# Optimization experiments

Measured on AMD Instinct MI355X. Metric: run time of the kernel, lower is better.

## Reference

```python
import jax, jax.numpy as jnp
import numpy as np

T = 1048576          # number of time steps in the trace
SIGMA_NUM = 8
EPSILON_NUM = 8
FEAT = 2 + SIGMA_NUM + EPSILON_NUM  # [t, r_obs, sigmas..., epsilons...]


def setup_inputs() -> dict:
    key = jax.random.key(0)
    ks = jax.random.split(key, 6)
    trace = jax.random.normal(ks[0], (T, FEAT), dtype=jnp.float32)
    # column 0 is time: sorted grid with small dt so the 1M-step recurrence stays bounded
    trace = trace.at[:, 0].set(jnp.arange(T, dtype=jnp.float32) * 1e-3)
    # column 1 row 0 is the initial rate; keep it positive-ish
    trace = trace.at[0, 1].set(0.05)
    sigma_W = jax.random.normal(ks[1], (1, SIGMA_NUM), dtype=jnp.float32) * 0.01
    sigma_b = jax.random.normal(ks[2], (1,), dtype=jnp.float32) * 0.01
    eps_W = jax.random.normal(ks[3], (1, EPSILON_NUM), dtype=jnp.float32) * 0.01
    k = jnp.abs(jax.random.normal(ks[4], (1,), dtype=jnp.float32)) * 0.1
    theta = jnp.abs(jax.random.normal(ks[5], (1,), dtype=jnp.float32)) * 0.05
    return {"trace_data": trace, "sigma_W": sigma_W, "sigma_b": sigma_b,
            "eps_W": eps_W, "k": k, "theta": theta}


def reference(trace_data, sigma_W, sigma_b, eps_W, k, theta):
    S, E = SIGMA_NUM, EPSILON_NUM
    t = trace_data[:, 0]
    dts = t[1:] - t[:-1]                                   # [T-1]
    # sigma/epsilon projections depend only on trace data -> vectorize outside scan
    sig = trace_data[:-1, 2:2 + S] @ sigma_W[0] + sigma_b[0]   # [T-1]
    eps = trace_data[:-1, 2 + S:2 + S + E] @ eps_W[0]          # [T-1]
    kk = k[0]
    th = theta[0]
    r0 = trace_data[0, 1]

    def step(r, x):
        dt, s, e = x
        ode = r + kk * (th - r) * dt
        sde = s * jnp.sqrt(jnp.abs(r * dt)) * e
        r_next = ode + sde
        return r_next, r_next

    _, r_predicts = jax.lax.scan(step, r0, (dts, sig, eps))   # [T-1]
    regs = 2.0 * kk * th - sig ** 2                           # [T-1]
    return r_predicts, regs, dts
```

## Files before the change

### kernel.cpp

```cpp
#include <hip/hip_runtime.h>
#include <math.h>

#define NSTEPS  1048575
#define NPAD    1048576
#define FEAT    18
#define CLEN    4
#define CHUNKS  (NPAD / CLEN)
#define K2B     256
#define K2T     1024

__global__ void prep_kernel(const float* __restrict__ trace,
                            const float* __restrict__ sW, const float* __restrict__ sb,
                            const float* __restrict__ eW, const float* __restrict__ kp,
                            const float* __restrict__ thp,
                            float2* __restrict__ dc, float* __restrict__ seeds,
                            float* __restrict__ out, unsigned int* __restrict__ cnt)
{
    int n = blockIdx.x * blockDim.x + threadIdx.x;
    if (n == 0) *cnt = 0;
    if (n >= NSTEPS) { dc[n] = make_float2(0.f, 0.f); return; }
    const float2* r2 = (const float2*)(trace + (long)n * FEAT);
    float2 e0 = r2[0], e1 = r2[1], e2 = r2[2], e3 = r2[3], e4 = r2[4];
    float2 e5 = r2[5], e6 = r2[6], e7 = r2[7], e8 = r2[8];
    float tn1 = trace[(long)(n + 1) * FEAT];
    float d = tn1 - e0.x;
    float sig = sb[0];
    sig = fmaf(e1.x, sW[0], sig); sig = fmaf(e1.y, sW[1], sig);
    sig = fmaf(e2.x, sW[2], sig); sig = fmaf(e2.y, sW[3], sig);
    sig = fmaf(e3.x, sW[4], sig); sig = fmaf(e3.y, sW[5], sig);
    sig = fmaf(e4.x, sW[6], sig); sig = fmaf(e4.y, sW[7], sig);
    float ep = 0.f;
    ep = fmaf(e5.x, eW[0], ep); ep = fmaf(e5.y, eW[1], ep);
    ep = fmaf(e6.x, eW[2], ep); ep = fmaf(e6.y, eW[3], ep);
    ep = fmaf(e7.x, eW[4], ep); ep = fmaf(e7.y, eW[5], ep);
    ep = fmaf(e8.x, eW[6], ep); ep = fmaf(e8.y, eW[7], ep);
    float k = kp[0], th = thp[0];
    dc[n] = make_float2(d, sig * ep * sqrtf(fabsf(d)));
    out[NSTEPS + n]     = fmaf(-sig, sig, 2.f * k * th);
    out[2 * NSTEPS + n] = d;
    if ((n & 3) == 0)
        seeds[n >> 2] = th + (trace[1] - th) * __expf(-k * (e0.x - trace[0]));
}

#define GSTEP(dd, cc) { \
    float a   = fmaf(-k, (dd), 1.f); \
    float b   = kth * (dd); \
    float ar  = fabsf(r); \
    float sq  = sqrtf(ar); \
    float inv = (ar > 1e-30f) ? rsqrtf(ar) : 0.f; \
    float g   = fmaf(0.5f * (cc), copysignf(inv, r), a); \
    r = fmaf((cc), sq, fmaf(a, r, b)); \
    P *= g; }

#define FSTEP(dd, cc) { \
    float a = fmaf(-k, (dd), 1.f); \
    float b = kth * (dd); \
    rr = fmaf((cc), sqrtf(fabsf(rr)), fmaf(a, rr, b)); }

__device__ __forceinline__ void wave_scan_affine(float& A, float& B, int lane) {
#pragma unroll
    for (int d = 1; d < 64; d <<= 1) {
        float pA = __shfl_up(A, d, 64);
        float pB = __shfl_up(B, d, 64);
        if (lane >= d) { B = fmaf(A, pB, B); A *= pA; }
    }
}

__global__ void __launch_bounds__(K2T) fused_pass(
    const float2* __restrict__ dc, const float* __restrict__ seeds,
    const float* __restrict__ trace,
    const float* __restrict__ kp, const float* __restrict__ thp,
    float* __restrict__ out,
    float* __restrict__ gA, float* __restrict__ gB,
    unsigned int* __restrict__ cnt)
{
    __shared__ float wAs[16], wBs[16];
    __shared__ float sgA[K2B], sgB[K2B];
    const int tid = threadIdx.x, lane = tid & 63, wid = tid >> 6, bid = blockIdx.x;
    const int c = bid * K2T + tid;
    const float k = kp[0], th = thp[0], kth = k * th;
    const float4 q0 = ((const float4*)dc)[2 * c];
    const float4 q1 = ((const float4*)dc)[2 * c + 1];
    const float s = seeds[c];

    float r = s, P = 1.f;
    GSTEP(q0.x, q0.y)
    GSTEP(q0.z, q0.w)
    GSTEP(q1.x, q1.y)
    GSTEP(q1.z, q1.w)
    float A = P, B = fmaf(-P, s, r);

    float iA = A, iB = B;
    wave_scan_affine(iA, iB, lane);
    if (lane == 63) { wAs[wid] = iA; wBs[wid] = iB; }
    __syncthreads();
    if (wid == 0) {
        float aA = (lane < 16) ? wAs[lane] : 1.f;
        float aB = (lane < 16) ? wBs[lane] : 0.f;
        wave_scan_affine(aA, aB, lane);
        if (lane < 16) { wAs[lane] = aA; wBs[lane] = aB; }
    }
    __syncthreads();
    float weA = 1.f, weB = 0.f;
    if (wid > 0) { weA = wAs[wid - 1]; weB = wBs[wid - 1]; }
    float eA = __shfl_up(iA, 1, 64), eB = __shfl_up(iB, 1, 64);
    if (lane == 0) { eA = 1.f; eB = 0.f; }
    float Ate = eA * weA;
    float Bte = fmaf(eA, weB, eB);

    if (tid == 0) {
        __hip_atomic_store(&gA[bid], wAs[15], __ATOMIC_RELAXED, __HIP_MEMORY_SCOPE_AGENT);
        __hip_atomic_store(&gB[bid], wBs[15], __ATOMIC_RELAXED, __HIP_MEMORY_SCOPE_AGENT);
        __hip_atomic_fetch_add(cnt, 1u, __ATOMIC_ACQ_REL, __HIP_MEMORY_SCOPE_AGENT);
        while (__hip_atomic_load(cnt, __ATOMIC_ACQUIRE, __HIP_MEMORY_SCOPE_AGENT) < K2B)
            __builtin_amdgcn_s_sleep(1);
    }
    __syncthreads();

    if (tid < K2B) {
        sgA[tid] = __hip_atomic_load(&gA[tid], __ATOMIC_RELAXED, __HIP_MEMORY_SCOPE_AGENT);
        sgB[tid] = __hip_atomic_load(&gB[tid], __ATOMIC_RELAXED, __HIP_MEMORY_SCOPE_AGENT);
    }
    __syncthreads();
    for (int d = 1; d < K2B; d <<= 1) {
        float pA = 1.f, pB = 0.f;
        bool act = (tid < K2B) && (tid >= d);
        if (act) { pA = sgA[tid - d]; pB = sgB[tid - d]; }
        __syncthreads();
        if (act) { sgB[tid] = fmaf(sgA[tid], pB, sgB[tid]); sgA[tid] *= pA; }
        __syncthreads();
    }
    float beA = 1.f, beB = 0.f;
    if (bid > 0) { beA = sgA[bid - 1]; beB = sgB[bid - 1]; }

    float FA = Ate * beA;
    float FB = fmaf(Ate, beB, Bte);
    float rr = fmaf(FA, trace[1], FB);
    float4 ov;
    FSTEP(q0.x, q0.y) ov.x = rr;
    FSTEP(q0.z, q0.w) ov.y = rr;
    FSTEP(q1.x, q1.y) ov.z = rr;
    FSTEP(q1.z, q1.w) ov.w = rr;
    int nb = 4 * c;
    if (nb + 4 <= NSTEPS) {
        *(float4*)(out + nb) = ov;
    } else {
        out[nb + 0] = ov.x;
        out[nb + 1] = ov.y;
        out[nb + 2] = ov.z;
    }
}

extern "C" void kernel_launch(void* const* d_in, const int* in_sizes, int n_in,
                              void* d_out, int out_size, void* d_ws, size_t ws_size,
                              hipStream_t stream)
{
    const float* trace = (const float*)d_in[0];
    const float* sW    = (const float*)d_in[1];
    const float* sb    = (const float*)d_in[2];
    const float* eW    = (const float*)d_in[3];
    const float* kp    = (const float*)d_in[4];
    const float* thp   = (const float*)d_in[5];
    float* out = (float*)d_out;

    float*        w     = (float*)d_ws;
    float2*       dc    = (float2*)w;
    float*        seeds = w + 2 * NPAD;
    float*        gA    = seeds + CHUNKS;
    float*        gB    = gA + K2B;
    unsigned int* cnt   = (unsigned int*)(gB + K2B);

    prep_kernel<<<NPAD / 256, 256, 0, stream>>>(trace, sW, sb, eW, kp, thp,
                                                dc, seeds, out, cnt);
    fused_pass<<<K2B, K2T, 0, stream>>>(dc, seeds, trace, kp, thp, out, gA, gB, cnt);
}
```

Baseline: 130.7 us.

## Fuse prep into scan kernel with double-buffered LDS staging of trace rows

```diff
diff --git a/kernel.cpp b/kernel.cpp
--- a/kernel.cpp
+++ b/kernel.cpp
@@ -2,44 +2,31 @@
 #include <math.h>
 
 #define NSTEPS  1048575
-#define NPAD    1048576
 #define FEAT    18
-#define CLEN    4
-#define CHUNKS  (NPAD / CLEN)
-#define K2B     256
-#define K2T     1024
-
-__global__ void prep_kernel(const float* __restrict__ trace,
-                            const float* __restrict__ sW, const float* __restrict__ sb,
-                            const float* __restrict__ eW, const float* __restrict__ kp,
-                            const float* __restrict__ thp,
-                            float2* __restrict__ dc, float* __restrict__ seeds,
-                            float* __restrict__ out, unsigned int* __restrict__ cnt)
+#define NB      256
+#define NT      1024
+#define RPB     (NT * 4)
+#define CROWS   NT
+#define NCHUNK  (RPB / CROWS)
+#define CF4     ((CROWS * FEAT) / 4)
+
+#define GLDS16(g, l) \
+    __builtin_amdgcn_global_load_lds((const __attribute__((address_space(1))) void*)(g), \
+                                     (__attribute__((address_space(3))) void*)(l), 16, 0, 0)
+
+__device__ __forceinline__ void stage_chunk(const float* __restrict__ trace,
+                                            long gbase, float* dst, int tid)
 {
-    int n = blockIdx.x * blockDim.x + threadIdx.x;
-    if (n == 0) *cnt = 0;
-    if (n >= NSTEPS) { dc[n] = make_float2(0.f, 0.f); return; }
-    const float2* r2 = (const float2*)(trace + (long)n * FEAT);
-    float2 e0 = r2[0], e1 = r2[1], e2 = r2[2], e3 = r2[3], e4 = r2[4];
-    float2 e5 = r2[5], e6 = r2[6], e7 = r2[7], e8 = r2[8];
-    float tn1 = trace[(long)(n + 1) * FEAT];
-    float d = tn1 - e0.x;
-    float sig = sb[0];
-    sig = fmaf(e1.x, sW[0], sig); sig = fmaf(e1.y, sW[1], sig);
-    sig = fmaf(e2.x, sW[2], sig); sig = fmaf(e2.y, sW[3], sig);
-    sig = fmaf(e3.x, sW[4], sig); sig = fmaf(e3.y, sW[5], sig);
-    sig = fmaf(e4.x, sW[6], sig); sig = fmaf(e4.y, sW[7], sig);
-    float ep = 0.f;
-    ep = fmaf(e5.x, eW[0], ep); ep = fmaf(e5.y, eW[1], ep);
-    ep = fmaf(e6.x, eW[2], ep); ep = fmaf(e6.y, eW[3], ep);
-    ep = fmaf(e7.x, eW[4], ep); ep = fmaf(e7.y, eW[5], ep);
-    ep = fmaf(e8.x, eW[6], ep); ep = fmaf(e8.y, eW[7], ep);
-    float k = kp[0], th = thp[0];
-    dc[n] = make_float2(d, sig * ep * sqrtf(fabsf(d)));
-    out[NSTEPS + n]     = fmaf(-sig, sig, 2.f * k * th);
-    out[2 * NSTEPS + n] = d;
-    if ((n & 3) == 0)
-        seeds[n >> 2] = th + (trace[1] - th) * __expf(-k * (e0.x - trace[0]));
+    const float4* src = (const float4*)(trace + gbase * FEAT);
+#pragma unroll
+    for (int r = 0; r < 4; ++r) {
+        int i = r * NT + tid;
+        GLDS16(src + i, dst + i * 4);
+    }
+    if (tid < (CF4 - 4 * NT)) {
+        int i = 4 * NT + tid;
+        GLDS16(src + i, dst + i * 4);
+    }
 }
 
 #define GSTEP(dd, cc) { \
@@ -66,31 +53,91 @@
     }
 }
 
-__global__ void __launch_bounds__(K2T) fused_pass(
-    const float2* __restrict__ dc, const float* __restrict__ seeds,
+__global__ void __launch_bounds__(NT) cir_fused(
     const float* __restrict__ trace,
-    const float* __restrict__ kp, const float* __restrict__ thp,
+    const float* __restrict__ sW, const float* __restrict__ sb,
+    const float* __restrict__ eW, const float* __restrict__ kp,
+    const float* __restrict__ thp,
     float* __restrict__ out,
     float* __restrict__ gA, float* __restrict__ gB,
     unsigned int* __restrict__ cnt)
 {
+    __shared__ __align__(16) float  buf[2][CROWS * FEAT];
+    __shared__ __align__(16) float2 dcl[CROWS];
     __shared__ float wAs[16], wBs[16];
-    __shared__ float sgA[K2B], sgB[K2B];
+    __shared__ float sgA[NB], sgB[NB];
+
     const int tid = threadIdx.x, lane = tid & 63, wid = tid >> 6, bid = blockIdx.x;
-    const int c = bid * K2T + tid;
+    const long blkrow = (long)bid * RPB;
+
+    stage_chunk(trace, blkrow, buf[0], tid);
+
     const float k = kp[0], th = thp[0], kth = k * th;
-    const float4 q0 = ((const float4*)dc)[2 * c];
-    const float4 q1 = ((const float4*)dc)[2 * c + 1];
-    const float s = seeds[c];
-
+    const float tkth2 = 2.f * kth;
+    const float sb0 = sb[0];
+    float sw[8], ew[8];
+#pragma unroll
+    for (int i = 0; i < 8; ++i) { sw[i] = sW[i]; ew[i] = eW[i]; }
+    const float t0 = trace[0], r0v = trace[1];
+
+    float4 q0 = make_float4(0.f, 0.f, 0.f, 0.f);
+    float4 q1 = make_float4(0.f, 0.f, 0.f, 0.f);
+    float tfirst = 0.f;
+
+    __syncthreads();
+
+    for (int ch = 0; ch < NCHUNK; ++ch) {
+        const float* B = buf[ch & 1];
+        if (ch + 1 < NCHUNK)
+            stage_chunk(trace, blkrow + (long)(ch + 1) * CROWS, buf[(ch + 1) & 1], tid);
+
+        long n = blkrow + (long)ch * CROWS + tid;
+        float dv = 0.f, cv = 0.f;
+        if (n < NSTEPS) {
+            const float* row = B + tid * FEAT;
+            float t  = row[0];
+            float tn = (tid < NT - 1) ? row[FEAT] : trace[(n + 1) * FEAT];
+            dv = tn - t;
+            const float2* f = (const float2*)(row + 2);
+            float2 a0 = f[0], a1 = f[1], a2 = f[2], a3 = f[3];
+            float2 b0 = f[4], b1 = f[5], b2 = f[6], b3 = f[7];
+            float sig = sb0;
+            sig = fmaf(a0.x, sw[0], sig); sig = fmaf(a0.y, sw[1], sig);
+            sig = fmaf(a1.x, sw[2], sig); sig = fmaf(a1.y, sw[3], sig);
+            sig = fmaf(a2.x, sw[4], sig); sig = fmaf(a2.y, sw[5], sig);
+            sig = fmaf(a3.x, sw[6], sig); sig = fmaf(a3.y, sw[7], sig);
+            float ep = 0.f;
+            ep = fmaf(b0.x, ew[0], ep); ep = fmaf(b0.y, ew[1], ep);
+            ep = fmaf(b1.x, ew[2], ep); ep = fmaf(b1.y, ew[3], ep);
+            ep = fmaf(b2.x, ew[4], ep); ep = fmaf(b2.y, ew[5], ep);
+            ep = fmaf(b3.x, ew[6], ep); ep = fmaf(b3.y, ew[7], ep);
+            cv = sig * ep * sqrtf(fabsf(dv));
+            out[NSTEPS + n]      = fmaf(-sig, sig, tkth2);
+            out[2L * NSTEPS + n] = dv;
+        }
+        dcl[tid] = make_float2(dv, cv);
+        __syncthreads();
+
+        if ((tid >> 8) == ch) {
+            int tr = tid & 255;
+            const float4* dq = (const float4*)dcl;
+            q0 = dq[2 * tr];
+            q1 = dq[2 * tr + 1];
+            tfirst = B[(4 * tr) * FEAT];
+        }
+        __syncthreads();
+    }
+
+    const int c = bid * NT + tid;
+    float s = th + (r0v - th) * __expf(-k * (tfirst - t0));
     float r = s, P = 1.f;
     GSTEP(q0.x, q0.y)
     GSTEP(q0.z, q0.w)
     GSTEP(q1.x, q1.y)
     GSTEP(q1.z, q1.w)
-    float A = P, B = fmaf(-P, s, r);
-
-    float iA = A, iB = B;
+    float A = P, Bv = fmaf(-P, s, r);
+
+    float iA = A, iB = Bv;
     wave_scan_affine(iA, iB, lane);
     if (lane == 63) { wAs[wid] = iA; wBs[wid] = iB; }
     __syncthreads();
@@ -112,19 +159,19 @@
         __hip_atomic_store(&gA[bid], wAs[15], __ATOMIC_RELAXED, __HIP_MEMORY_SCOPE_AGENT);
         __hip_atomic_store(&gB[bid], wBs[15], __ATOMIC_RELAXED, __HIP_MEMORY_SCOPE_AGENT);
         __hip_atomic_fetch_add(cnt, 1u, __ATOMIC_ACQ_REL, __HIP_MEMORY_SCOPE_AGENT);
-        while (__hip_atomic_load(cnt, __ATOMIC_ACQUIRE, __HIP_MEMORY_SCOPE_AGENT) < K2B)
+        while (__hip_atomic_load(cnt, __ATOMIC_ACQUIRE, __HIP_MEMORY_SCOPE_AGENT) < NB)
             __builtin_amdgcn_s_sleep(1);
     }
     __syncthreads();
 
-    if (tid < K2B) {
+    if (tid < NB) {
         sgA[tid] = __hip_atomic_load(&gA[tid], __ATOMIC_RELAXED, __HIP_MEMORY_SCOPE_AGENT);
         sgB[tid] = __hip_atomic_load(&gB[tid], __ATOMIC_RELAXED, __HIP_MEMORY_SCOPE_AGENT);
     }
     __syncthreads();
-    for (int d = 1; d < K2B; d <<= 1) {
+    for (int d = 1; d < NB; d <<= 1) {
         float pA = 1.f, pB = 0.f;
-        bool act = (tid < K2B) && (tid >= d);
+        bool act = (tid < NB) && (tid >= d);
         if (act) { pA = sgA[tid - d]; pB = sgB[tid - d]; }
         __syncthreads();
         if (act) { sgB[tid] = fmaf(sgA[tid], pB, sgB[tid]); sgA[tid] *= pA; }
@@ -135,7 +182,7 @@
 
     float FA = Ate * beA;
     float FB = fmaf(Ate, beB, Bte);
-    float rr = fmaf(FA, trace[1], FB);
+    float rr = fmaf(FA, r0v, FB);
     float4 ov;
     FSTEP(q0.x, q0.y) ov.x = rr;
     FSTEP(q0.z, q0.w) ov.y = rr;
@@ -163,14 +210,10 @@
     const float* thp   = (const float*)d_in[5];
     float* out = (float*)d_out;
 
-    float*        w     = (float*)d_ws;
-    float2*       dc    = (float2*)w;
-    float*        seeds = w + 2 * NPAD;
-    float*        gA    = seeds + CHUNKS;
-    float*        gB    = gA + K2B;
-    unsigned int* cnt   = (unsigned int*)(gB + K2B);
-
-    prep_kernel<<<NPAD / 256, 256, 0, stream>>>(trace, sW, sb, eW, kp, thp,
-                                                dc, seeds, out, cnt);
-    fused_pass<<<K2B, K2T, 0, stream>>>(dc, seeds, trace, kp, thp, out, gA, gB, cnt);
-}
+    float*        gA  = (float*)d_ws;
+    float*        gB  = gA + NB;
+    unsigned int* cnt = (unsigned int*)(gB + NB);
+
+    hipMemsetAsync(cnt, 0, sizeof(unsigned int), stream);
+    cir_fused<<<NB, NT, 0, stream>>>(trace, sW, sb, eW, kp, thp, out, gA, gB, cnt);
+}
```

Result: slower. 146.9 us (+12.4%).

## Fuse prep into scan kernel, reading trace rows directly with vector loads

Applied to the files above, without the earlier changes.

```diff
diff --git a/kernel.cpp b/kernel.cpp
--- a/kernel.cpp
+++ b/kernel.cpp
@@ -1,46 +1,11 @@
 #include <hip/hip_runtime.h>
 #include <math.h>
 
-#define NSTEPS  1048575
-#define NPAD    1048576
-#define FEAT    18
-#define CLEN    4
-#define CHUNKS  (NPAD / CLEN)
-#define K2B     256
-#define K2T     1024
-
-__global__ void prep_kernel(const float* __restrict__ trace,
-                            const float* __restrict__ sW, const float* __restrict__ sb,
-                            const float* __restrict__ eW, const float* __restrict__ kp,
-                            const float* __restrict__ thp,
-                            float2* __restrict__ dc, float* __restrict__ seeds,
-                            float* __restrict__ out, unsigned int* __restrict__ cnt)
-{
-    int n = blockIdx.x * blockDim.x + threadIdx.x;
-    if (n == 0) *cnt = 0;
-    if (n >= NSTEPS) { dc[n] = make_float2(0.f, 0.f); return; }
-    const float2* r2 = (const float2*)(trace + (long)n * FEAT);
-    float2 e0 = r2[0], e1 = r2[1], e2 = r2[2], e3 = r2[3], e4 = r2[4];
-    float2 e5 = r2[5], e6 = r2[6], e7 = r2[7], e8 = r2[8];
-    float tn1 = trace[(long)(n + 1) * FEAT];
-    float d = tn1 - e0.x;
-    float sig = sb[0];
-    sig = fmaf(e1.x, sW[0], sig); sig = fmaf(e1.y, sW[1], sig);
-    sig = fmaf(e2.x, sW[2], sig); sig = fmaf(e2.y, sW[3], sig);
-    sig = fmaf(e3.x, sW[4], sig); sig = fmaf(e3.y, sW[5], sig);
-    sig = fmaf(e4.x, sW[6], sig); sig = fmaf(e4.y, sW[7], sig);
-    float ep = 0.f;
-    ep = fmaf(e5.x, eW[0], ep); ep = fmaf(e5.y, eW[1], ep);
-    ep = fmaf(e6.x, eW[2], ep); ep = fmaf(e6.y, eW[3], ep);
-    ep = fmaf(e7.x, eW[4], ep); ep = fmaf(e7.y, eW[5], ep);
-    ep = fmaf(e8.x, eW[6], ep); ep = fmaf(e8.y, eW[7], ep);
-    float k = kp[0], th = thp[0];
-    dc[n] = make_float2(d, sig * ep * sqrtf(fabsf(d)));
-    out[NSTEPS + n]     = fmaf(-sig, sig, 2.f * k * th);
-    out[2 * NSTEPS + n] = d;
-    if ((n & 3) == 0)
-        seeds[n >> 2] = th + (trace[1] - th) * __expf(-k * (e0.x - trace[0]));
-}
+#define NSTEPS   1048575
+#define FEAT     18
+#define NB       256
+#define NT       1024
+#define NTHREADS (NB * NT)
 
 #define GSTEP(dd, cc) { \
     float a   = fmaf(-k, (dd), 1.f); \
@@ -57,6 +22,19 @@
     float b = kth * (dd); \
     rr = fmaf((cc), sqrtf(fabsf(rr)), fmaf(a, rr, b)); }
 
+#define ROWCOEF(S0,S1,S2,S3,S4,S5,S6,S7, E0,E1,E2,E3,E4,E5,E6,E7, dv, sigv, cvv) { \
+    float sig_ = sb0; \
+    sig_ = fmaf((S0), sw0, sig_); sig_ = fmaf((S1), sw1, sig_); \
+    sig_ = fmaf((S2), sw2, sig_); sig_ = fmaf((S3), sw3, sig_); \
+    sig_ = fmaf((S4), sw4, sig_); sig_ = fmaf((S5), sw5, sig_); \
+    sig_ = fmaf((S6), sw6, sig_); sig_ = fmaf((S7), sw7, sig_); \
+    float ep_ = 0.f; \
+    ep_ = fmaf((E0), ew0, ep_); ep_ = fmaf((E1), ew1, ep_); \
+    ep_ = fmaf((E2), ew2, ep_); ep_ = fmaf((E3), ew3, ep_); \
+    ep_ = fmaf((E4), ew4, ep_); ep_ = fmaf((E5), ew5, ep_); \
+    ep_ = fmaf((E6), ew6, ep_); ep_ = fmaf((E7), ew7, ep_); \
+    (sigv) = sig_; (cvv) = sig_ * ep_ * sqrtf(fabsf(dv)); }
+
 __device__ __forceinline__ void wave_scan_affine(float& A, float& B, int lane) {
 #pragma unroll
     for (int d = 1; d < 64; d <<= 1) {
@@ -66,31 +44,79 @@
     }
 }
 
-__global__ void __launch_bounds__(K2T) fused_pass(
-    const float2* __restrict__ dc, const float* __restrict__ seeds,
+__global__ void __launch_bounds__(NT) cir_fused(
     const float* __restrict__ trace,
-    const float* __restrict__ kp, const float* __restrict__ thp,
+    const float* __restrict__ sW, const float* __restrict__ sb,
+    const float* __restrict__ eW, const float* __restrict__ kp,
+    const float* __restrict__ thp,
     float* __restrict__ out,
     float* __restrict__ gA, float* __restrict__ gB,
     unsigned int* __restrict__ cnt)
 {
     __shared__ float wAs[16], wBs[16];
-    __shared__ float sgA[K2B], sgB[K2B];
+    __shared__ float sgA[NB], sgB[NB];
+
     const int tid = threadIdx.x, lane = tid & 63, wid = tid >> 6, bid = blockIdx.x;
-    const int c = bid * K2T + tid;
-    const float k = kp[0], th = thp[0], kth = k * th;
-    const float4 q0 = ((const float4*)dc)[2 * c];
-    const float4 q1 = ((const float4*)dc)[2 * c + 1];
-    const float s = seeds[c];
-
+    const long c = (long)bid * NT + tid;
+
+    const float4* __restrict__ src = (const float4*)trace + c * 18;
+    float4 v0  = src[0],  v1  = src[1],  v2  = src[2],  v3  = src[3],  v4  = src[4];
+    float4 v5  = src[5],  v6  = src[6],  v7  = src[7],  v8  = src[8];
+    float4 v9  = src[9],  v10 = src[10], v11 = src[11], v12 = src[12], v13 = src[13];
+    float4 v14 = src[14], v15 = src[15], v16 = src[16], v17 = src[17];
+
+    const float k = kp[0], th = thp[0], kth = k * th, tkth2 = 2.f * kth;
+    const float sb0 = sb[0];
+    const float sw0 = sW[0], sw1 = sW[1], sw2 = sW[2], sw3 = sW[3];
+    const float sw4 = sW[4], sw5 = sW[5], sw6 = sW[6], sw7 = sW[7];
+    const float ew0 = eW[0], ew1 = eW[1], ew2 = eW[2], ew3 = eW[3];
+    const float ew4 = eW[4], ew5 = eW[5], ew6 = eW[6], ew7 = eW[7];
+    const float t0g = trace[0], r0v = trace[1];
+
+    float tnext = __shfl_down(v0.x, 1, 64);
+    if (lane == 63)
+        tnext = (c + 1 < (long)NTHREADS) ? trace[(c * 4 + 4) * FEAT] : 0.f;
+
+    float d0 = v4.z  - v0.x;
+    float d1 = v9.x  - v4.z;
+    float d2 = v13.z - v9.x;
+    float d3 = tnext - v13.z;
+    float sig0, c0v, sig1, c1v, sig2, c2v, sig3, c3v;
+    ROWCOEF(v0.z,v0.w,v1.x,v1.y,v1.z,v1.w,v2.x,v2.y,
+            v2.z,v2.w,v3.x,v3.y,v3.z,v3.w,v4.x,v4.y, d0, sig0, c0v)
+    ROWCOEF(v5.x,v5.y,v5.z,v5.w,v6.x,v6.y,v6.z,v6.w,
+            v7.x,v7.y,v7.z,v7.w,v8.x,v8.y,v8.z,v8.w, d1, sig1, c1v)
+    ROWCOEF(v9.z,v9.w,v10.x,v10.y,v10.z,v10.w,v11.x,v11.y,
+            v11.z,v11.w,v12.x,v12.y,v12.z,v12.w,v13.x,v13.y, d2, sig2, c2v)
+    ROWCOEF(v14.x,v14.y,v14.z,v14.w,v15.x,v15.y,v15.z,v15.w,
+            v16.x,v16.y,v16.z,v16.w,v17.x,v17.y,v17.z,v17.w, d3, sig3, c3v)
+
+    const long n0 = c * 4;
+    if (n0 + 4 > NSTEPS) { d3 = 0.f; c3v = 0.f; }
+
+    out[NSTEPS + n0 + 0] = fmaf(-sig0, sig0, tkth2);
+    out[NSTEPS + n0 + 1] = fmaf(-sig1, sig1, tkth2);
+    out[NSTEPS + n0 + 2] = fmaf(-sig2, sig2, tkth2);
+    out[2L * NSTEPS + n0 + 0] = d0;
+    out[2L * NSTEPS + n0 + 1] = d1;
+    out[2L * NSTEPS + n0 + 2] = d2;
+    if (n0 + 4 <= NSTEPS) {
+        out[NSTEPS + n0 + 3] = fmaf(-sig3, sig3, tkth2);
+        out[2L * NSTEPS + n0 + 3] = d3;
+    }
+
+    const float4 q0 = make_float4(d0, c0v, d1, c1v);
+    const float4 q1 = make_float4(d2, c2v, d3, c3v);
+
+    float s = th + (r0v - th) * __expf(-k * (v0.x - t0g));
     float r = s, P = 1.f;
     GSTEP(q0.x, q0.y)
     GSTEP(q0.z, q0.w)
     GSTEP(q1.x, q1.y)
     GSTEP(q1.z, q1.w)
-    float A = P, B = fmaf(-P, s, r);
-
-    float iA = A, iB = B;
+    float A = P, Bv = fmaf(-P, s, r);
+
+    float iA = A, iB = Bv;
     wave_scan_affine(iA, iB, lane);
     if (lane == 63) { wAs[wid] = iA; wBs[wid] = iB; }
     __syncthreads();
@@ -112,36 +138,40 @@
         __hip_atomic_store(&gA[bid], wAs[15], __ATOMIC_RELAXED, __HIP_MEMORY_SCOPE_AGENT);
         __hip_atomic_store(&gB[bid], wBs[15], __ATOMIC_RELAXED, __HIP_MEMORY_SCOPE_AGENT);
         __hip_atomic_fetch_add(cnt, 1u, __ATOMIC_ACQ_REL, __HIP_MEMORY_SCOPE_AGENT);
-        while (__hip_atomic_load(cnt, __ATOMIC_ACQUIRE, __HIP_MEMORY_SCOPE_AGENT) < K2B)
+        while (__hip_atomic_load(cnt, __ATOMIC_ACQUIRE, __HIP_MEMORY_SCOPE_AGENT) < NB)
             __builtin_amdgcn_s_sleep(1);
     }
     __syncthreads();
 
-    if (tid < K2B) {
-        sgA[tid] = __hip_atomic_load(&gA[tid], __ATOMIC_RELAXED, __HIP_MEMORY_SCOPE_AGENT);
-        sgB[tid] = __hip_atomic_load(&gB[tid], __ATOMIC_RELAXED, __HIP_MEMORY_SCOPE_AGENT);
-    }
-    __syncthreads();
-    for (int d = 1; d < K2B; d <<= 1) {
-        float pA = 1.f, pB = 0.f;
-        bool act = (tid < K2B) && (tid >= d);
-        if (act) { pA = sgA[tid - d]; pB = sgB[tid - d]; }
-        __syncthreads();
-        if (act) { sgB[tid] = fmaf(sgA[tid], pB, sgB[tid]); sgA[tid] *= pA; }
-        __syncthreads();
-    }
+    float bAv = 1.f, bBv = 0.f;
+    if (tid < NB) {
+        bAv = __hip_atomic_load(&gA[tid], __ATOMIC_RELAXED, __HIP_MEMORY_SCOPE_AGENT);
+        bBv = __hip_atomic_load(&gB[tid], __ATOMIC_RELAXED, __HIP_MEMORY_SCOPE_AGENT);
+    }
+    if (wid < NB / 64) {
+        wave_scan_affine(bAv, bBv, lane);
+        if (lane == 63) { wAs[wid] = bAv; wBs[wid] = bBv; }
+    }
+    __syncthreads();
+    if (tid < NB) {
+        float Pa = 1.f, Pb = 0.f;
+        for (int w = 0; w < wid; ++w) { Pb = fmaf(wAs[w], Pb, wBs[w]); Pa *= wAs[w]; }
+        sgA[tid] = bAv * Pa;
+        sgB[tid] = fmaf(bAv, Pb, bBv);
+    }
+    __syncthreads();
     float beA = 1.f, beB = 0.f;
     if (bid > 0) { beA = sgA[bid - 1]; beB = sgB[bid - 1]; }
 
     float FA = Ate * beA;
     float FB = fmaf(Ate, beB, Bte);
-    float rr = fmaf(FA, trace[1], FB);
+    float rr = fmaf(FA, r0v, FB);
     float4 ov;
     FSTEP(q0.x, q0.y) ov.x = rr;
     FSTEP(q0.z, q0.w) ov.y = rr;
     FSTEP(q1.x, q1.y) ov.z = rr;
     FSTEP(q1.z, q1.w) ov.w = rr;
-    int nb = 4 * c;
+    long nb = 4 * c;
     if (nb + 4 <= NSTEPS) {
         *(float4*)(out + nb) = ov;
     } else {
@@ -163,14 +193,10 @@
     const float* thp   = (const float*)d_in[5];
     float* out = (float*)d_out;
 
-    float*        w     = (float*)d_ws;
-    float2*       dc    = (float2*)w;
-    float*        seeds = w + 2 * NPAD;
-    float*        gA    = seeds + CHUNKS;
-    float*        gB    = gA + K2B;
-    unsigned int* cnt   = (unsigned int*)(gB + K2B);
-
-    prep_kernel<<<NPAD / 256, 256, 0, stream>>>(trace, sW, sb, eW, kp, thp,
-                                                dc, seeds, out, cnt);
-    fused_pass<<<K2B, K2T, 0, stream>>>(dc, seeds, trace, kp, thp, out, gA, gB, cnt);
+    float*        gA  = (float*)d_ws;
+    float*        gB  = gA + NB;
+    unsigned int* cnt = (unsigned int*)(gB + NB);
+
+    hipMemsetAsync(cnt, 0, sizeof(unsigned int), stream);
+    cir_fused<<<NB, NT, 0, stream>>>(trace, sW, sb, eW, kp, thp, out, gA, gB, cnt);
 }
```

New measurement: 167.5 us. 28.1% more time.
